# Kernel optimization log

Measured on AMD Instinct MI355X. Metric: run time of the kernel, lower is better.

Reference implementation:

```python
import jax, jax.numpy as jnp
import numpy as np

B, S, H = 2, 2048, 2048
N_HEADS = 16
HEAD_DIM = H // N_HEADS


def setup_inputs() -> dict:
    key = jax.random.key(0)
    ks = jax.random.split(key, 9)
    s = 1.0 / np.sqrt(H)
    inp = {
        "x": jax.random.normal(ks[0], (B, S, H), dtype=jnp.float32),
        "wq": jax.random.uniform(ks[1], (H, H), jnp.float32, -s, s),
        "bq": jnp.zeros((H,), jnp.float32),
        "wk": jax.random.uniform(ks[2], (H, H), jnp.float32, -s, s),
        "bk": jnp.zeros((H,), jnp.float32),
        "wv": jax.random.uniform(ks[3], (H, H), jnp.float32, -s, s),
        "bv": jnp.zeros((H,), jnp.float32),
        "wo": jax.random.uniform(ks[4], (H, H), jnp.float32, -s, s),
        "bo": jnp.zeros((H,), jnp.float32),
    }
    return inp


def reference(x, wq, bq, wk, bk, wv, bv, wo, bo):
    bsz, seq_len, hidden = x.shape
    scale = HEAD_DIM ** -0.5
    # projections -> [b, h, s, d]
    def proj(w, b):
        y = jnp.einsum("bsh,oh->bso", x, w) + b
        return y.reshape(bsz, seq_len, N_HEADS, HEAD_DIM).transpose(0, 2, 1, 3)
    q = proj(wq, bq)
    k = proj(wk, bk)
    v = proj(wv, bv)
    scores = jnp.einsum("bhqd,bhkd->bhqk", q, k) * scale
    causal = jnp.tril(jnp.ones((seq_len, seq_len), dtype=bool))
    scores = jnp.where(causal, scores, -jnp.inf)
    attn = jax.nn.softmax(scores, axis=-1)
    out = jnp.einsum("bhqk,bhkd->bhqd", attn, v)
    out = out.transpose(0, 2, 1, 3).reshape(bsz, seq_len, hidden)
    return jnp.einsum("bsh,oh->bso", out, wo) + bo
```

## Files before the change

### kernel.cpp

```cpp
#include <hip/hip_runtime.h>
#include <hip/hip_bf16.h>
#include <cstdint>
#include <cstddef>

#define BATCH 2
#define S_LEN 2048
#define HID   2048
#define NH    16
#define HD    128
#define GK    2048
#define NT    (GK / 64)
#define NIT   (NT / 2)
#define ATT_TILES (32 * NH * BATCH)

typedef short bf16x8 __attribute__((ext_vector_type(8)));
typedef float f32x4  __attribute__((ext_vector_type(4)));

__device__ inline unsigned short f2bf(float f) {
    unsigned int u = __float_as_uint(f);
    unsigned int r = (u + 0x7fffu + ((u >> 16) & 1u)) >> 16;
    return (unsigned short)r;
}

__global__ __launch_bounds__(256) void conv_f32_bf16(const float* __restrict__ src,
                                                     unsigned short* __restrict__ dst,
                                                     long n) {
    long i = ((long)blockIdx.x * 256 + threadIdx.x) * 8;
    if (i >= n) return;
    const float4 a = *(const float4*)(src + i);
    const float4 b = *(const float4*)(src + i + 4);
    union { unsigned short u[8]; bf16x8 v; } o;
    o.u[0] = f2bf(a.x); o.u[1] = f2bf(a.y); o.u[2] = f2bf(a.z); o.u[3] = f2bf(a.w);
    o.u[4] = f2bf(b.x); o.u[5] = f2bf(b.y); o.u[6] = f2bf(b.z); o.u[7] = f2bf(b.w);
    *(bf16x8*)(dst + i) = o.v;
}

__global__ __launch_bounds__(256) void conv4_f32_bf16(const float* __restrict__ s0,
                                                      const float* __restrict__ s1,
                                                      const float* __restrict__ s2,
                                                      const float* __restrict__ s3,
                                                      unsigned short* __restrict__ d0,
                                                      unsigned short* __restrict__ d1,
                                                      unsigned short* __restrict__ d2,
                                                      unsigned short* __restrict__ d3,
                                                      long n) {
    const int z = blockIdx.y;
    const float* src = (z == 0) ? s0 : (z == 1) ? s1 : (z == 2) ? s2 : s3;
    unsigned short* dst = (z == 0) ? d0 : (z == 1) ? d1 : (z == 2) ? d2 : d3;
    long i = ((long)blockIdx.x * 256 + threadIdx.x) * 8;
    if (i >= n) return;
    const float4 a = *(const float4*)(src + i);
    const float4 b = *(const float4*)(src + i + 4);
    union { unsigned short u[8]; bf16x8 v; } o;
    o.u[0] = f2bf(a.x); o.u[1] = f2bf(a.y); o.u[2] = f2bf(a.z); o.u[3] = f2bf(a.w);
    o.u[4] = f2bf(b.x); o.u[5] = f2bf(b.y); o.u[6] = f2bf(b.z); o.u[7] = f2bf(b.w);
    *(bf16x8*)(dst + i) = o.v;
}

__global__ void zero_int(int* p) { *p = 0; }


#define STAGE(DU, SRC, KT, H) do {                                            \
    const unsigned short* _s0 = (SRC) + (size_t)((H) * 128) * GK + (KT) * 64; \
    __builtin_amdgcn_global_load_lds(                                         \
        (const __attribute__((address_space(1))) void*)_s0,                   \
        (__attribute__((address_space(3))) void*)(Sm + (DU) + (H) * 8192 + sdst), \
        16, 0, 0);                                                            \
    __builtin_amdgcn_global_load_lds(                                         \
        (const __attribute__((address_space(1))) void*)(_s0 + (size_t)64 * GK), \
        (__attribute__((address_space(3))) void*)(Sm + (DU) + (H) * 8192 + 4096 + sdst), \
        16, 0, 0);                                                            \
} while (0)

#define READ_A(D, HI) do { _Pragma("unroll")                                  \
    for (int mi = 0; mi < 2; ++mi) {                                          \
        const int r_ = wm * 64 + ((HI) * 2 + mi) * 16 + ln;                   \
        a[(HI)*2+mi][0] = *(const bf16x8*)&Sm[(D) * 24576 + r_ * 64 + sw0];   \
        a[(HI)*2+mi][1] = *(const bf16x8*)&Sm[(D) * 24576 + r_ * 64 + sw1];   \
    } } while (0)

#define READ_B(D, HI) do { _Pragma("unroll")                                  \
    for (int ni = 0; ni < 2; ++ni) {                                          \
        const int r_ = wn * 64 + ((HI) * 2 + ni) * 16 + ln;                   \
        b[(HI)*2+ni][0] = *(const bf16x8*)&Sm[(D) * 24576 + 16384 + r_ * 64 + sw0]; \
        b[(HI)*2+ni][1] = *(const bf16x8*)&Sm[(D) * 24576 + 16384 + r_ * 64 + sw1]; \
    } } while (0)

#define MFMA8(MA, NA) do { _Pragma("unroll")                                  \
    for (int mi = 0; mi < 2; ++mi) _Pragma("unroll")                          \
    for (int ni = 0; ni < 2; ++ni) _Pragma("unroll")                          \
    for (int ks = 0; ks < 2; ++ks)                                            \
        acc[(MA)*2+mi][(NA)*2+ni] = __builtin_amdgcn_mfma_f32_16x16x32_bf16(  \
            a[(MA)*2+mi][ks], b[(NA)*2+ni][ks], acc[(MA)*2+mi][(NA)*2+ni], 0, 0, 0); \
} while (0)

#define PH_BEGIN  __builtin_amdgcn_s_barrier();                               \
                  asm volatile("s_waitcnt lgkmcnt(0)" ::: "memory");          \
                  __builtin_amdgcn_s_setprio(1)
#define PH_END    __builtin_amdgcn_s_setprio(0); __builtin_amdgcn_s_barrier()
#define PH_END_V2 __builtin_amdgcn_s_setprio(0);                              \
                  asm volatile("s_waitcnt vmcnt(2)" ::: "memory");            \
                  __builtin_amdgcn_s_barrier()
#define PH_END_V4 __builtin_amdgcn_s_setprio(0);                              \
                  asm volatile("s_waitcnt vmcnt(4)" ::: "memory");            \
                  __builtin_amdgcn_s_barrier()

__device__ __forceinline__ void gemm256_core(const unsigned short* __restrict__ A,
                                             const unsigned short* __restrict__ Bw,
                                             const float* __restrict__ bias,
                                             void* __restrict__ Cout,
                                             int mode, int M0, int N0,
                                             unsigned short* Sm) {
    const int tid  = threadIdx.x;
    const int lane = tid & 63;
    const int wave = tid >> 6;
    const int ln = lane & 15, g = lane >> 4;
    const int wm = wave & 3, wn = wave >> 2;

    const int strow = tid >> 3;
    const int stcol = (((tid & 7) ^ ((tid >> 3) & 7)) << 3);
    const unsigned short* gA = A  + (size_t)(M0 + strow) * GK + stcol;
    const unsigned short* gB = Bw + (size_t)(N0 + strow) * GK + stcol;
    const int sdst = wave * 512;

    const int sw0 = ((g    ) ^ (ln & 7)) << 3;
    const int sw1 = ((g + 4) ^ (ln & 7)) << 3;

    f32x4 acc[4][4];
#pragma unroll
    for (int i = 0; i < 4; ++i)
#pragma unroll
        for (int j = 0; j < 4; ++j) acc[i][j] = (f32x4){0.f, 0.f, 0.f, 0.f};
    bf16x8 a[4][2], b[4][2];

    STAGE(0,     gA, 0, 0); STAGE(0,     gA, 0, 1);
    STAGE(16384, gB, 0, 0);
    STAGE(24576, gA, 1, 0); STAGE(24576, gA, 1, 1);
    asm volatile("s_waitcnt vmcnt(4)" ::: "memory");
    __builtin_amdgcn_s_barrier();

    for (int it = 0; it < NIT; ++it) {
        const int kt1 = 2 * it + 1;
        const int kt2 = (2 * it + 2 < NT) ? 2 * it + 2 : NT - 1;
        const int kt3 = (2 * it + 3 < NT) ? 2 * it + 3 : NT - 1;
        READ_A(0, 0); READ_B(0, 0);
        STAGE(40960, gB, kt1, 0);
        PH_BEGIN; MFMA8(0, 0); PH_END;
        READ_B(0, 1);
        PH_BEGIN; MFMA8(0, 1); PH_END;
        READ_A(0, 1);
        STAGE(16384, gB, kt2, 0);
        PH_BEGIN; MFMA8(1, 0); PH_END;
        PH_BEGIN; MFMA8(1, 1); PH_END_V2;
        READ_A(1, 0); READ_B(1, 0);
        STAGE(0, gA, kt2, 0);
        PH_BEGIN; MFMA8(0, 0); PH_END;
        READ_B(1, 1);
        STAGE(0, gA, kt2, 1);
        PH_BEGIN; MFMA8(0, 1); PH_END;
        READ_A(1, 1);
        PH_BEGIN; MFMA8(1, 0); PH_END;
        STAGE(24576, gA, kt3, 0); STAGE(24576, gA, kt3, 1);
        PH_BEGIN; MFMA8(1, 1); PH_END_V4;
    }
    asm volatile("s_waitcnt vmcnt(0)" ::: "memory");
    __syncthreads();

    if (mode == 0) {
        const int bb = M0 >> 11;
        const int sb = M0 & (S_LEN - 1);
        const int h  = N0 >> 7;
#pragma unroll
        for (int nf = 0; nf < 4; ++nf) {
            const int d = wn * 64 + nf * 16 + ln;
            const float bn = bias[N0 + d];
            unsigned short* dst = (unsigned short*)Cout +
                (((size_t)(bb * NH + h) * S_LEN + sb + wm * 64) * HD + d);
#pragma unroll
            for (int mf = 0; mf < 4; ++mf)
#pragma unroll
                for (int r = 0; r < 4; ++r)
                    dst[(size_t)(mf * 16 + g * 4 + r) * HD] = f2bf(acc[mf][nf][r] + bn);
        }
    } else if (mode == 2) {
        float* dst = (float*)Cout;
#pragma unroll
        for (int nf = 0; nf < 4; ++nf) {
            const int n = N0 + wn * 64 + nf * 16 + ln;
            const float bn = bias[n];
#pragma unroll
            for (int mf = 0; mf < 4; ++mf)
#pragma unroll
                for (int r = 0; r < 4; ++r) {
                    const int m = M0 + wm * 64 + mf * 16 + g * 4 + r;
                    dst[(size_t)m * HID + n] = acc[mf][nf][r] + bn;
                }
        }
    } else {
        const int bb = M0 >> 11;
        const int sb = M0 & (S_LEN - 1);
        const int h  = N0 >> 7;
#pragma unroll
        for (int p = 0; p < 2; ++p) {
            if ((wm >> 1) == p) {
#pragma unroll
                for (int nf = 0; nf < 4; ++nf) {
                    const int dl = wn * 64 + nf * 16 + ln;
                    const float bn = bias[N0 + dl];
#pragma unroll
                    for (int mf = 0; mf < 4; ++mf) {
                        const int sl = (wm & 1) * 64 + mf * 16 + g * 4;
                        const int cs = (sl >> 3) ^ (dl & 15);
                        union { unsigned short u[4]; unsigned long long q; } pk;
#pragma unroll
                        for (int r = 0; r < 4; ++r) pk.u[r] = f2bf(acc[mf][nf][r] + bn);
                        *(unsigned long long*)&Sm[dl * 128 + cs * 8 + (sl & 7)] = pk.q;
                    }
                }
            }
            __syncthreads();
            {
                const int dl = tid >> 2;
                unsigned short* dst = (unsigned short*)Cout +
                    ((size_t)(bb * NH + h) * HD + dl) * S_LEN + sb + p * 128;
#pragma unroll
                for (int jj = 0; jj < 4; ++jj) {
                    const int sc = (tid & 3) + jj * 4;
                    const int cs = sc ^ (dl & 15);
                    *(bf16x8*)(dst + sc * 8) = *(const bf16x8*)&Sm[dl * 128 + cs * 8];
                }
            }
            __syncthreads();
        }
    }
}

__device__ __forceinline__ void xcd_remap(int& M0, int& N0) {
    const int f = blockIdx.y * gridDim.x + blockIdx.x;
    const int c = f & 7, j = f >> 3;
    const int nx_ = 2 * c + (j & 1);
    const int ny_ = j >> 1;
    M0 = ny_ * 256;
    N0 = nx_ * 128;
}

__global__ __launch_bounds__(512, 2) void gemm_qkv256(
        const unsigned short* __restrict__ A,
        const unsigned short* __restrict__ w0, const unsigned short* __restrict__ w1,
        const unsigned short* __restrict__ w2,
        const float* __restrict__ b0, const float* __restrict__ b1,
        const float* __restrict__ b2,
        void* o0, void* o1, void* o2) {
    extern __shared__ __align__(16) unsigned short Sm[];
    const int z = blockIdx.z;
    const unsigned short* Bw = (z == 0) ? w0 : (z == 1) ? w1 : w2;
    const float* bias = (z == 0) ? b0 : (z == 1) ? b1 : b2;
    void* Cout = (z == 0) ? o0 : (z == 1) ? o1 : o2;
    int M0, N0; xcd_remap(M0, N0);
    gemm256_core(A, Bw, bias, Cout, (z == 2) ? 1 : 0, M0, N0, Sm);
}

__global__ __launch_bounds__(512, 2) void gemm_out256(
        const unsigned short* __restrict__ A, const unsigned short* __restrict__ Bw,
        const float* __restrict__ bias, float* __restrict__ Cout) {
    extern __shared__ __align__(16) unsigned short Sm[];
    int M0, N0; xcd_remap(M0, N0);
    gemm256_core(A, Bw, bias, Cout, 2, M0, N0, Sm);
}

__global__ __launch_bounds__(256, 2) void attn_kernel(const unsigned short* __restrict__ Q,
                                                      const unsigned short* __restrict__ Kk,
                                                      const unsigned short* __restrict__ Vt,
                                                      unsigned short* __restrict__ O,
                                                      int* __restrict__ ticket) {
    __shared__ __align__(16) unsigned short Ks[2 * 64 * 128];
    __shared__ __align__(16) unsigned short Vs[2 * 128 * 64];
    __shared__ __align__(16) unsigned short Pl[4][16 * 72];
    __shared__ int tsh;
    const int tid = threadIdx.x;
    const int lane = tid & 63;
    const int wave = tid >> 6;
    const int g = lane >> 4, ln = lane & 15;
    const float scale2 = 0.08838834764831845f * 1.4426950408889634f;
    const bf16x8 ones_v = {0x3F80, 0x3F80, 0x3F80, 0x3F80, 0x3F80, 0x3F80, 0x3F80, 0x3F80};

    const int kcol = ((tid & 15) ^ ((tid >> 4) & 15)) * 8;
    const int vcol = ((tid & 7) ^ ((tid >> 3) & 7)) * 8;

    for (;;) {
        if (tid == 0) tsh = atomicAdd(ticket, 1);
        __syncthreads();
        const int t = tsh;
        if (t >= ATT_TILES) break;
        const int qt = 31 - (t >> 5);
        const int bh = t & 31;
        const int qbase = qt * 64 + wave * 16;

        const unsigned short* Qp = Q  + (size_t)bh * S_LEN * HD;
        const unsigned short* Kp = Kk + (size_t)bh * S_LEN * HD;
        const unsigned short* Vp = Vt + (size_t)bh * HD * S_LEN;

        bf16x8 aq[4];
#pragma unroll
        for (int dc = 0; dc < 4; ++dc)
            aq[dc] = *(const bf16x8*)&Qp[(size_t)(qbase + ln) * HD + dc * 32 + g * 8];

        f32x4 acc[9];
#pragma unroll
        for (int i = 0; i < 9; ++i) acc[i] = (f32x4){0.f, 0.f, 0.f, 0.f};

#pragma unroll
        for (int i = 0; i < 4; ++i) {
            const unsigned short* gk = Kp + (size_t)(i * 16 + (tid >> 4)) * HD + kcol;
            __builtin_amdgcn_global_load_lds(
                (const __attribute__((address_space(1))) void*)gk,
                (__attribute__((address_space(3))) void*)(Ks + i * 2048 + wave * 512),
                16, 0, 0);
        }
#pragma unroll
        for (int i = 0; i < 4; ++i) {
            const unsigned short* gv = Vp + (size_t)(i * 32 + (tid >> 3)) * S_LEN + vcol;
            __builtin_amdgcn_global_load_lds(
                (const __attribute__((address_space(1))) void*)gv,
                (__attribute__((address_space(3))) void*)(Vs + i * 2048 + wave * 512),
                16, 0, 0);
        }

        for (int kt = 0; kt <= qt; ++kt) {
            const int cur = kt & 1;
            const bool do_stage = (kt + 1 <= qt);
            if (do_stage) {
                const int kb2 = (kt + 1) * 64;
                const int nb  = (kt + 1) & 1;
                unsigned short* kdst = Ks + nb * 8192 + wave * 512;
                unsigned short* vdst = Vs + nb * 8192 + wave * 512;
#pragma unroll
                for (int i = 0; i < 4; ++i) {
                    const unsigned short* gk = Kp + (size_t)(kb2 + i * 16 + (tid >> 4)) * HD + kcol;
                    __builtin_amdgcn_global_load_lds(
                        (const __attribute__((address_space(1))) void*)gk,
                        (__attribute__((address_space(3))) void*)(kdst + i * 2048),
                        16, 0, 0);
                }
#pragma unroll
                for (int i = 0; i < 4; ++i) {
                    const unsigned short* gv = Vp + (size_t)(i * 32 + (tid >> 3)) * S_LEN + kb2 + vcol;
                    __builtin_amdgcn_global_load_lds(
                        (const __attribute__((address_space(1))) void*)gv,
                        (__attribute__((address_space(3))) void*)(vdst + i * 2048),
                        16, 0, 0);
                }
            }
            if (kt == 0 || !do_stage) {
                asm volatile("s_waitcnt vmcnt(0)" ::: "memory");
            } else {
                asm volatile("s_waitcnt vmcnt(8)" ::: "memory");
            }
            __builtin_amdgcn_s_barrier();

            const int kbuf = cur * 8192;
            f32x4 sc[4];
            __builtin_amdgcn_s_setprio(1);
#pragma unroll
            for (int nc = 0; nc < 4; ++nc) {
                sc[nc] = (f32x4){0.f, 0.f, 0.f, 0.f};
#pragma unroll
                for (int dc = 0; dc < 4; ++dc) {
                    bf16x8 bk = *(const bf16x8*)&Ks[kbuf + (nc * 16 + ln) * 128 + ((dc * 4 + g) ^ ln) * 8];
                    sc[nc] = __builtin_amdgcn_mfma_f32_16x16x32_bf16(aq[dc], bk, sc[nc], 0, 0, 0);
                }
            }
            __builtin_amdgcn_s_setprio(0);
            const bool diag = (kt == qt);
#pragma unroll
            for (int nc = 0; nc < 4; ++nc)
#pragma unroll
                for (int r = 0; r < 4; ++r) {
                    float pv = __builtin_amdgcn_exp2f(sc[nc][r] * scale2);
                    if (diag && (nc * 16 + ln > wave * 16 + g * 4 + r)) pv = 0.f;
                    Pl[wave][(g * 4 + r) * 72 + nc * 16 + ln] = f2bf(pv);
                }
            __builtin_amdgcn_s_setprio(1);
#pragma unroll
            for (int kc = 0; kc < 2; ++kc) {
                bf16x8 ap = *(const bf16x8*)&Pl[wave][ln * 72 + kc * 32 + g * 8];
#pragma unroll
                for (int d2 = 0; d2 < 8; ++d2) {
                    bf16x8 bv = *(const bf16x8*)&Vs[kbuf + (d2 * 16 + ln) * 64 + ((kc * 4 + g) ^ (ln & 7)) * 8];
                    acc[d2] = __builtin_amdgcn_mfma_f32_16x16x32_bf16(ap, bv, acc[d2], 0, 0, 0);
                }
                acc[8] = __builtin_amdgcn_mfma_f32_16x16x32_bf16(ap, ones_v, acc[8], 0, 0, 0);
            }
            __builtin_amdgcn_s_setprio(0);
            __builtin_amdgcn_s_barrier();
        }
        const int b = bh >> 4, h = bh & 15;
        float inv[4];
#pragma unroll
        for (int r = 0; r < 4; ++r) inv[r] = 1.0f / acc[8][r];
#pragma unroll
        for (int d2 = 0; d2 < 8; ++d2)
#pragma unroll
            for (int r = 0; r < 4; ++r) {
                const int row = qbase + g * 4 + r;
                const int col = h * HD + d2 * 16 + ln;
                O[((size_t)b * S_LEN + row) * HID + col] = f2bf(acc[d2][r] * inv[r]);
            }
    }
}

extern "C" void kernel_launch(void* const* d_in, const int* in_sizes, int n_in,
                              void* d_out, int out_size, void* d_ws, size_t ws_size,
                              hipStream_t stream) {
    const float* x  = (const float*)d_in[0];
    const float* wq = (const float*)d_in[1];
    const float* bq = (const float*)d_in[2];
    const float* wk = (const float*)d_in[3];
    const float* bk = (const float*)d_in[4];
    const float* wv = (const float*)d_in[5];
    const float* bv = (const float*)d_in[6];
    const float* wo = (const float*)d_in[7];
    const float* bo = (const float*)d_in[8];
    float* out = (float*)d_out;

    const long nx = (long)BATCH * S_LEN * HID;
    const long nw = (long)HID * HID;

    char* p = (char*)d_ws;
    unsigned short* xb  = (unsigned short*)p; p += nx * 2;
    unsigned short* wqb = (unsigned short*)p; p += nw * 2;
    unsigned short* wkb = (unsigned short*)p; p += nw * 2;
    unsigned short* wvb = (unsigned short*)p; p += nw * 2;
    unsigned short* wob = (unsigned short*)p; p += nw * 2;
    unsigned short* Qb  = (unsigned short*)p; p += nx * 2;
    unsigned short* Kb  = (unsigned short*)p; p += nx * 2;
    unsigned short* Vtb = (unsigned short*)p; p += nx * 2;
    unsigned short* Ob  = (unsigned short*)p; p += nx * 2;
    int* ticket = (int*)p;

    conv_f32_bf16<<<(int)(nx / 8 / 256), 256, 0, stream>>>(x, xb, nx);
    dim3 cgrid((unsigned)(nw / 8 / 256), 4);
    conv4_f32_bf16<<<cgrid, 256, 0, stream>>>(wq, wk, wv, wo, wqb, wkb, wvb, wob, nw);
    zero_int<<<1, 1, 0, stream>>>(ticket);

    const int M = BATCH * S_LEN;
    dim3 qkvgrid(HID / 128, M / 256, 3);
    gemm_qkv256<<<qkvgrid, 512, 98304, stream>>>(xb, wqb, wkb, wvb, bq, bk, bv,
                                                 Qb, Kb, Vtb);

    attn_kernel<<<512, 256, 0, stream>>>(Qb, Kb, Vtb, Ob, ticket);

    dim3 ogrid(HID / 128, M / 256);
    gemm_out256<<<ogrid, 512, 98304, stream>>>(Ob, wob, bo, out);
}
```

Baseline: 371.7 us.

## Restructure GEMM main loop into four-phase register double-buffered schedule

Rewrites the bf16 GEMM inner loop to keep full A fragments for even and odd K-tiles in separate register sets and to prefetch the next B half while the current MFMAs run. Per-iteration barriers drop from sixteen to four, with vmcnt(0) waits at two points. It also removes the XCD-aware block index remap and goes back to plain blockIdx tiling. This cuts synchronization and LDS-read stalls but raises register pressure, and losing the remap may hurt L2 locality across XCDs.

```diff
diff --git a/kernel.cpp b/kernel.cpp
--- a/kernel.cpp
+++ b/kernel.cpp
@@ -72,38 +72,32 @@
         16, 0, 0);                                                            \
 } while (0)
 
-#define READ_A(D, HI) do { _Pragma("unroll")                                  \
-    for (int mi = 0; mi < 2; ++mi) {                                          \
-        const int r_ = wm * 64 + ((HI) * 2 + mi) * 16 + ln;                   \
-        a[(HI)*2+mi][0] = *(const bf16x8*)&Sm[(D) * 24576 + r_ * 64 + sw0];   \
-        a[(HI)*2+mi][1] = *(const bf16x8*)&Sm[(D) * 24576 + r_ * 64 + sw1];   \
+#define READ_AF(D, AB) do { _Pragma("unroll")                                 \
+    for (int mi = 0; mi < 4; ++mi) {                                          \
+        const int r_ = wm * 64 + mi * 16 + ln;                                \
+        AB[mi][0] = *(const bf16x8*)&Sm[(D) * 24576 + r_ * 64 + sw0];         \
+        AB[mi][1] = *(const bf16x8*)&Sm[(D) * 24576 + r_ * 64 + sw1];         \
     } } while (0)
 
-#define READ_B(D, HI) do { _Pragma("unroll")                                  \
+#define READ_BH(D, BB, HH) do { _Pragma("unroll")                             \
     for (int ni = 0; ni < 2; ++ni) {                                          \
-        const int r_ = wn * 64 + ((HI) * 2 + ni) * 16 + ln;                   \
-        b[(HI)*2+ni][0] = *(const bf16x8*)&Sm[(D) * 24576 + 16384 + r_ * 64 + sw0]; \
-        b[(HI)*2+ni][1] = *(const bf16x8*)&Sm[(D) * 24576 + 16384 + r_ * 64 + sw1]; \
+        const int r_ = wn * 64 + ((HH) * 2 + ni) * 16 + ln;                   \
+        BB[ni][0] = *(const bf16x8*)&Sm[(D) * 24576 + 16384 + r_ * 64 + sw0]; \
+        BB[ni][1] = *(const bf16x8*)&Sm[(D) * 24576 + 16384 + r_ * 64 + sw1]; \
     } } while (0)
 
-#define MFMA8(MA, NA) do { _Pragma("unroll")                                  \
-    for (int mi = 0; mi < 2; ++mi) _Pragma("unroll")                          \
+#define MFMA_H(AB, BB, HH) do { _Pragma("unroll")                             \
+    for (int mi = 0; mi < 4; ++mi) _Pragma("unroll")                          \
     for (int ni = 0; ni < 2; ++ni) _Pragma("unroll")                          \
     for (int ks = 0; ks < 2; ++ks)                                            \
-        acc[(MA)*2+mi][(NA)*2+ni] = __builtin_amdgcn_mfma_f32_16x16x32_bf16(  \
-            a[(MA)*2+mi][ks], b[(NA)*2+ni][ks], acc[(MA)*2+mi][(NA)*2+ni], 0, 0, 0); \
+        acc[mi][(HH)*2+ni] = __builtin_amdgcn_mfma_f32_16x16x32_bf16(         \
+            AB[mi][ks], BB[ni][ks], acc[mi][(HH)*2+ni], 0, 0, 0);             \
 } while (0)
 
-#define PH_BEGIN  __builtin_amdgcn_s_barrier();                               \
-                  asm volatile("s_waitcnt lgkmcnt(0)" ::: "memory");          \
-                  __builtin_amdgcn_s_setprio(1)
-#define PH_END    __builtin_amdgcn_s_setprio(0); __builtin_amdgcn_s_barrier()
-#define PH_END_V2 __builtin_amdgcn_s_setprio(0);                              \
-                  asm volatile("s_waitcnt vmcnt(2)" ::: "memory");            \
-                  __builtin_amdgcn_s_barrier()
-#define PH_END_V4 __builtin_amdgcn_s_setprio(0);                              \
-                  asm volatile("s_waitcnt vmcnt(4)" ::: "memory");            \
-                  __builtin_amdgcn_s_barrier()
+#define PRIO1 __builtin_amdgcn_s_setprio(1)
+#define PRIO0 __builtin_amdgcn_s_setprio(0)
+#define BAR   __builtin_amdgcn_s_barrier()
+#define VM0   asm volatile("s_waitcnt vmcnt(0)" ::: "memory")
 
 __device__ __forceinline__ void gemm256_core(const unsigned short* __restrict__ A,
                                              const unsigned short* __restrict__ Bw,
@@ -131,37 +125,37 @@
     for (int i = 0; i < 4; ++i)
 #pragma unroll
         for (int j = 0; j < 4; ++j) acc[i][j] = (f32x4){0.f, 0.f, 0.f, 0.f};
-    bf16x8 a[4][2], b[4][2];
+    bf16x8 aE[4][2], aO[4][2], bA[2][2], bB[2][2];
 
     STAGE(0,     gA, 0, 0); STAGE(0,     gA, 0, 1);
     STAGE(16384, gB, 0, 0);
     STAGE(24576, gA, 1, 0); STAGE(24576, gA, 1, 1);
     asm volatile("s_waitcnt vmcnt(4)" ::: "memory");
-    __builtin_amdgcn_s_barrier();
+    BAR;
+    READ_AF(0, aE); READ_BH(0, bA, 0);
 
     for (int it = 0; it < NIT; ++it) {
         const int kt1 = 2 * it + 1;
         const int kt2 = (2 * it + 2 < NT) ? 2 * it + 2 : NT - 1;
         const int kt3 = (2 * it + 3 < NT) ? 2 * it + 3 : NT - 1;
-        READ_A(0, 0); READ_B(0, 0);
-        STAGE(40960, gB, kt1, 0);
-        PH_BEGIN; MFMA8(0, 0); PH_END;
-        READ_B(0, 1);
-        PH_BEGIN; MFMA8(0, 1); PH_END;
-        READ_A(0, 1);
+        BAR;
+        STAGE(24576 + 16384, gB, kt1, 0);
+        READ_BH(0, bB, 1);
+        PRIO1; MFMA_H(aE, bA, 0); PRIO0;
+        VM0;
+        BAR;
+        STAGE(0, gA, kt2, 0); STAGE(0, gA, kt2, 1);
+        READ_AF(1, aO); READ_BH(1, bA, 0);
+        PRIO1; MFMA_H(aE, bB, 1); PRIO0;
+        BAR;
         STAGE(16384, gB, kt2, 0);
-        PH_BEGIN; MFMA8(1, 0); PH_END;
-        PH_BEGIN; MFMA8(1, 1); PH_END_V2;
-        READ_A(1, 0); READ_B(1, 0);
-        STAGE(0, gA, kt2, 0);
-        PH_BEGIN; MFMA8(0, 0); PH_END;
-        READ_B(1, 1);
-        STAGE(0, gA, kt2, 1);
-        PH_BEGIN; MFMA8(0, 1); PH_END;
-        READ_A(1, 1);
-        PH_BEGIN; MFMA8(1, 0); PH_END;
+        READ_BH(1, bB, 1);
+        PRIO1; MFMA_H(aO, bA, 0); PRIO0;
+        VM0;
+        BAR;
         STAGE(24576, gA, kt3, 0); STAGE(24576, gA, kt3, 1);
-        PH_BEGIN; MFMA8(1, 1); PH_END_V4;
+        READ_AF(0, aE); READ_BH(0, bA, 0);
+        PRIO1; MFMA_H(aO, bB, 1); PRIO0;
     }
     asm volatile("s_waitcnt vmcnt(0)" ::: "memory");
     __syncthreads();
@@ -233,15 +227,6 @@
             __syncthreads();
         }
     }
-}
-
-__device__ __forceinline__ void xcd_remap(int& M0, int& N0) {
-    const int f = blockIdx.y * gridDim.x + blockIdx.x;
-    const int c = f & 7, j = f >> 3;
-    const int nx_ = 2 * c + (j & 1);
-    const int ny_ = j >> 1;
-    M0 = ny_ * 256;
-    N0 = nx_ * 128;
 }
 
 __global__ __launch_bounds__(512, 2) void gemm_qkv256(
@@ -256,16 +241,15 @@
     const unsigned short* Bw = (z == 0) ? w0 : (z == 1) ? w1 : w2;
     const float* bias = (z == 0) ? b0 : (z == 1) ? b1 : b2;
     void* Cout = (z == 0) ? o0 : (z == 1) ? o1 : o2;
-    int M0, N0; xcd_remap(M0, N0);
-    gemm256_core(A, Bw, bias, Cout, (z == 2) ? 1 : 0, M0, N0, Sm);
+    gemm256_core(A, Bw, bias, Cout, (z == 2) ? 1 : 0,
+                 blockIdx.y * 256, blockIdx.x * 128, Sm);
 }
 
 __global__ __launch_bounds__(512, 2) void gemm_out256(
         const unsigned short* __restrict__ A, const unsigned short* __restrict__ Bw,
         const float* __restrict__ bias, float* __restrict__ Cout) {
     extern __shared__ __align__(16) unsigned short Sm[];
-    int M0, N0; xcd_remap(M0, N0);
-    gemm256_core(A, Bw, bias, Cout, 2, M0, N0, Sm);
+    gemm256_core(A, Bw, bias, Cout, 2, blockIdx.y * 256, blockIdx.x * 128, Sm);
 }
 
 __global__ __launch_bounds__(256, 2) void attn_kernel(const unsigned short* __restrict__ Q,
```

Result: no change. 378.9 us (+1.9%).
